# Performance work log

Hardware: AMD Instinct MI355X
Metric: run time of the kernel (lower is better)

## Reference

```python
import jax, jax.numpy as jnp
from jax import lax
import numpy as np

DIM = 256
QK = 256          # qk_dim defaults to dim
HEADS = 8
NWIN = 7
TOPK = 4
KS = 3            # side_dwconv


def setup_inputs() -> dict:
    key = jax.random.key(0)
    ks = jax.random.split(key, 8)
    B, H, W = 1, 112, 112
    s = lambda d: 1.0 / np.sqrt(d)
    return {
        "x": jax.random.normal(ks[0], (B, H, W, DIM), jnp.float32),
        # fused qkv linear: dim -> qk + qk + dim
        "w_qkv": jax.random.normal(ks[1], (DIM, 2 * QK + DIM), jnp.float32) * s(DIM),
        "b_qkv": jnp.zeros((2 * QK + DIM,), jnp.float32),
        # output projection
        "w_o": jax.random.normal(ks[2], (DIM, DIM), jnp.float32) * s(DIM),
        "b_o": jnp.zeros((DIM,), jnp.float32),
        # depthwise 3x3 lepe conv (HWIO with I=1, groups=dim)
        "lepe_w": jax.random.normal(ks[3], (KS, KS, 1, DIM), jnp.float32) * s(KS * KS),
        "lepe_b": jnp.zeros((DIM,), jnp.float32),
    }


def _win2img(t, B, H, W, c):
    # (B, p2, h, w, c) windows -> (B, H, W, c) image
    hw, ww = H // NWIN, W // NWIN
    t = t.reshape(B, NWIN, NWIN, hw, ww, c)
    return t.transpose(0, 1, 3, 2, 4, 5).reshape(B, H, W, c)


def reference(x, w_qkv, b_qkv, w_o, b_o, lepe_w, lepe_b):
    B, H, W, C = x.shape
    hw, ww = H // NWIN, W // NWIN
    p2, w2 = NWIN * NWIN, hw * ww
    hd_q, hd_v = QK // HEADS, DIM // HEADS
    scale = QK ** (-0.5)

    # partition into windows: (B, p2, hw, ww, C)
    xp = x.reshape(B, NWIN, hw, NWIN, ww, C).transpose(0, 1, 3, 2, 4, 5)
    xp = xp.reshape(B, p2, hw, ww, C)

    qkv = xp @ w_qkv + b_qkv
    q, kv = qkv[..., :QK], qkv[..., QK:]          # (B,p2,hw,ww,QK), (...,QK+DIM)

    q_pix = q.reshape(B, p2, w2, QK)
    kv_pix = kv.reshape(B, p2, w2, QK + DIM)      # identity kv_down

    # region-level routing (detached in original since diff_routing=False)
    q_win = lax.stop_gradient(q.mean((2, 3)))     # (B,p2,QK)
    k_win = lax.stop_gradient(kv[..., :QK].mean((2, 3)))
    logit = (q_win * scale) @ jnp.swapaxes(k_win, -1, -2)   # (B,p2,p2)
    top_logit, top_idx = lax.top_k(logit, TOPK)             # (B,p2,TOPK)
    r_weight = jax.nn.softmax(top_logit, axis=-1)           # unused: mul_weight='none'

    # gather top-k regions' KV: (B, p2, TOPK, w2, QK+DIM)
    kv_sel = jax.vmap(lambda kvb, idxb: kvb[idxb])(kv_pix, top_idx)

    k_sel = kv_sel[..., :QK].reshape(B, p2, TOPK * w2, HEADS, hd_q)
    v_sel = kv_sel[..., QK:].reshape(B, p2, TOPK * w2, HEADS, hd_v)
    qh = q_pix.reshape(B, p2, w2, HEADS, hd_q)

    attn = jnp.einsum('bpqhc,bpkhc->bphqk', qh * scale, k_sel)
    attn = jax.nn.softmax(attn, axis=-1)
    out = jnp.einsum('bphqk,bpkhc->bpqhc', attn, v_sel).reshape(B, p2, hw, ww, DIM)
    out = _win2img(out, B, H, W, DIM)

    # lepe: depthwise conv over v in image layout
    v_img = _win2img(kv[..., QK:], B, H, W, DIM)
    lepe = lax.conv_general_dilated(
        v_img, lepe_w, (1, 1), 'SAME',
        dimension_numbers=('NHWC', 'HWIO', 'NHWC'),
        feature_group_count=DIM) + lepe_b

    return (out + lepe) @ w_o + b_o
```

## Files before the change

kernel.cpp:

```cpp
#include <hip/hip_runtime.h>
#include <math.h>


typedef __bf16 bf16x8 __attribute__((ext_vector_type(8)));
typedef __bf16 bf16x4 __attribute__((ext_vector_type(4)));
typedef float f32x4 __attribute__((ext_vector_type(4)));

__global__ __launch_bounds__(64)
void pack1(const float* __restrict__ x, const float* __restrict__ w_qkv,
           const float* __restrict__ w_o, __bf16* __restrict__ xbf,
           __bf16* __restrict__ wtq, __bf16* __restrict__ wto) {
    const int b = blockIdx.x;
    const int t = threadIdx.x;
    if (b < 12544) {
        int p = b >> 8, pix = b & 255;
        int hh = (p / 7) * 16 + (pix >> 4);
        int ww = (p % 7) * 16 + (pix & 15);
        const float* src = x + ((size_t)(hh * 112 + ww)) * 256 + t * 4;
        float4 v = *(const float4*)src;
        bf16x4 o;
        o[0] = (__bf16)v.x; o[1] = (__bf16)v.y; o[2] = (__bf16)v.z; o[3] = (__bf16)v.w;
        *(bf16x4*)(xbf + (size_t)b * 256 + t * 4) = o;
    } else if (b < 12544 + 768) {
        int n = b - 12544;
        int k = t * 4;
        bf16x4 o;
        o[0] = (__bf16)w_qkv[(k + 0) * 768 + n];
        o[1] = (__bf16)w_qkv[(k + 1) * 768 + n];
        o[2] = (__bf16)w_qkv[(k + 2) * 768 + n];
        o[3] = (__bf16)w_qkv[(k + 3) * 768 + n];
        *(bf16x4*)(wtq + (size_t)n * 256 + k) = o;
    } else {
        int n = b - 12544 - 768;
        int k = t * 4;
        bf16x4 o;
        o[0] = (__bf16)w_o[(k + 0) * 256 + n];
        o[1] = (__bf16)w_o[(k + 1) * 256 + n];
        o[2] = (__bf16)w_o[(k + 2) * 256 + n];
        o[3] = (__bf16)w_o[(k + 3) * 256 + n];
        *(bf16x4*)(wto + (size_t)n * 256 + k) = o;
    }
}

template<int QKV>
__global__ __launch_bounds__(256)
void gemm_bf16(const __bf16* __restrict__ A,
               const __bf16* __restrict__ Wt,
               const float* __restrict__ bias,
               float* __restrict__ C, int N,
               __bf16* __restrict__ Qp,
               __bf16* __restrict__ Kp,
               __bf16* __restrict__ vbf,
               __bf16* __restrict__ Vt) {
    const int t = threadIdx.x & 63;
    const int wv = threadIdx.x >> 6;
    const int l16 = t & 15, quad = t >> 4;
    const int m0 = blockIdx.x * 64;
    const int n0 = blockIdx.y * 128 + wv * 32;

    __shared__ __bf16 Vs[128][72];

    f32x4 acc[2][4];
#pragma unroll
    for (int km = 0; km < 2; km++)
#pragma unroll
        for (int nt = 0; nt < 4; nt++) acc[km][nt] = (f32x4){0.f, 0.f, 0.f, 0.f};

#pragma unroll
    for (int ks = 0; ks < 8; ks++) {
        bf16x8 Af[2], Bf[4];
#pragma unroll
        for (int km = 0; km < 2; km++)
            Af[km] = *(const bf16x8*)(Wt + (size_t)(n0 + km * 16 + l16) * 256 + ks * 32 + quad * 8);
#pragma unroll
        for (int nt = 0; nt < 4; nt++)
            Bf[nt] = *(const bf16x8*)(A + (size_t)(m0 + nt * 16 + l16) * 256 + ks * 32 + quad * 8);
#pragma unroll
        for (int km = 0; km < 2; km++)
#pragma unroll
            for (int nt = 0; nt < 4; nt++)
                acc[km][nt] = __builtin_amdgcn_mfma_f32_16x16x32_bf16(
                    Af[km], Bf[nt], acc[km][nt], 0, 0, 0);
    }

#pragma unroll
    for (int km = 0; km < 2; km++) {
        const int n = n0 + km * 16 + quad * 4;
        float4 b4 = *(const float4*)(bias + n);
#pragma unroll
        for (int nt = 0; nt < 4; nt++) {
            const int m = m0 + nt * 16 + l16;
            float v0 = acc[km][nt][0] + b4.x;
            float v1 = acc[km][nt][1] + b4.y;
            float v2 = acc[km][nt][2] + b4.z;
            float v3 = acc[km][nt][3] + b4.w;
            if (QKV == 0) {
                float4 o = {v0, v1, v2, v3};
                *(float4*)(C + (size_t)m * N + n) = o;
            } else {
                const int p = m >> 8, pix = m & 255;
                if (n0 < 256) {
                    const float s = 1.4426950408889634f / 16.0f;
                    int h = n >> 5, cc = n & 31;
                    bf16x4 o;
                    o[0] = (__bf16)(v0 * s); o[1] = (__bf16)(v1 * s);
                    o[2] = (__bf16)(v2 * s); o[3] = (__bf16)(v3 * s);
                    *(bf16x4*)(Qp + ((size_t)((p * 8 + h) * 256 + pix)) * 32 + cc) = o;
                } else if (n0 < 512) {
                    int n2 = n - 256;
                    int h = n2 >> 5, cc = n2 & 31;
                    bf16x4 o;
                    o[0] = (__bf16)v0; o[1] = (__bf16)v1;
                    o[2] = (__bf16)v2; o[3] = (__bf16)v3;
                    *(bf16x4*)(Kp + ((size_t)((p * 8 + h) * 256 + pix)) * 32 + cc) = o;
                } else {
                    int n2 = n - 512;
                    int imgrow = ((p / 7) * 16 + (pix >> 4)) * 112 + (p % 7) * 16 + (pix & 15);
                    bf16x4 o;
                    o[0] = (__bf16)v0; o[1] = (__bf16)v1;
                    o[2] = (__bf16)v2; o[3] = (__bf16)v3;
                    *(bf16x4*)(vbf + (size_t)imgrow * 256 + n2) = o;
                    const int cbase = wv * 32 + km * 16 + quad * 4;
                    const int pb = nt * 16 + l16;
                    Vs[cbase + 0][pb] = o[0];
                    Vs[cbase + 1][pb] = o[1];
                    Vs[cbase + 2][pb] = o[2];
                    Vs[cbase + 3][pb] = o[3];
                }
            }
        }
    }

    if (QKV == 1 && blockIdx.y >= 4) {
        __syncthreads();
        const int p_ = m0 >> 8, qt_ = (m0 >> 6) & 3;
        const int vb = blockIdx.y * 128 - 512;
#pragma unroll
        for (int rep = 0; rep < 4; rep++) {
            int id = rep * 256 + threadIdx.x;
            int row = id >> 3, c8 = (id & 7) * 8;
            int hh = (vb + row) >> 5, c32 = (vb + row) & 31;
            bf16x8 val = *(const bf16x8*)&Vs[row][c8];
            *(bf16x8*)(Vt + ((size_t)((p_ * 8 + hh) * 32 + c32)) * 256 + qt_ * 64 + c8) = val;
        }
    }
}

__global__ __launch_bounds__(256)
void win_means(const __bf16* __restrict__ Qp,
               const __bf16* __restrict__ Kp,
               float* __restrict__ q_win, float* __restrict__ k_win) {
    const int b = blockIdx.x;
    const int p = b >> 3, h = b & 7;
    const int t = threadIdx.x;
    const int c8 = (t & 3) * 8;
    const int r0 = t >> 2;
    float aq[8], ak[8];
#pragma unroll
    for (int j = 0; j < 8; j++) { aq[j] = 0.f; ak[j] = 0.f; }
#pragma unroll
    for (int rg = 0; rg < 4; rg++) {
        const int r = rg * 64 + r0;
        bf16x8 q = *(const bf16x8*)(Qp + ((size_t)(b * 256 + r)) * 32 + c8);
        bf16x8 k = *(const bf16x8*)(Kp + ((size_t)(b * 256 + r)) * 32 + c8);
#pragma unroll
        for (int j = 0; j < 8; j++) { aq[j] += (float)q[j]; ak[j] += (float)k[j]; }
    }
    __shared__ float Sq[256][8], Sk[256][8];
#pragma unroll
    for (int j = 0; j < 8; j++) { Sq[t][j] = aq[j]; Sk[t][j] = ak[j]; }
    __syncthreads();
    if (t < 32) {
        const int grp = t >> 3, cj = t & 7;
        float sq = 0.f, sk = 0.f;
        for (int i = 0; i < 64; i++) {
            sq += Sq[i * 4 + grp][cj];
            sk += Sk[i * 4 + grp][cj];
        }
        q_win[p * 256 + h * 32 + t] = sq * (1.f / 256.f);
        k_win[p * 256 + h * 32 + t] = sk * (1.f / 256.f);
    }
}

__global__ __launch_bounds__(64)
void routing_topk(const float* __restrict__ q_win,
                  const float* __restrict__ k_win,
                  int* __restrict__ top_idx) {
    const int r = blockIdx.x;
    const int j = threadIdx.x;
    __shared__ float vals[64];

    float d = -1e30f;
    if (j < 49) {
        const float4* qp = (const float4*)(q_win + r * 256);
        const float4* kp = (const float4*)(k_win + j * 256);
        float s = 0.f;
#pragma unroll
        for (int c = 0; c < 64; c++) {
            float4 a = qp[c], b = kp[c];
            s += a.x * b.x + a.y * b.y + a.z * b.z + a.w * b.w;
        }
        d = s;
    }
    vals[j] = d;
    __syncthreads();
    if (j == 0) {
        float bv0 = -1e30f, bv1 = -1e30f, bv2 = -1e30f, bv3 = -1e30f;
        int bi0 = 0, bi1 = 0, bi2 = 0, bi3 = 0;
        for (int q = 0; q < 49; q++) {
            float v = vals[q];
            if (v > bv0) {
                bv3 = bv2; bi3 = bi2; bv2 = bv1; bi2 = bi1; bv1 = bv0; bi1 = bi0;
                bv0 = v; bi0 = q;
            } else if (v > bv1) {
                bv3 = bv2; bi3 = bi2; bv2 = bv1; bi2 = bi1; bv1 = v; bi1 = q;
            } else if (v > bv2) {
                bv3 = bv2; bi3 = bi2; bv2 = v; bi2 = q;
            } else if (v > bv3) {
                bv3 = v; bi3 = q;
            }
        }
        top_idx[r * 4 + 0] = bi0;
        top_idx[r * 4 + 1] = bi1;
        top_idx[r * 4 + 2] = bi2;
        top_idx[r * 4 + 3] = bi3;
    }
}

#define PLDS_PITCH 68
#define HALO_PITCH 36

__global__ __launch_bounds__(256)
void attn_mfma(const __bf16* __restrict__ Qp,
               const __bf16* __restrict__ Kp,
               const __bf16* __restrict__ Vt,
               const int* __restrict__ top_idx,
               const __bf16* __restrict__ vbf,
               const float* __restrict__ lw,
               const float* __restrict__ lb,
               __bf16* __restrict__ prebf) {
    const int bb = blockIdx.x;
    const int qt = bb / 392;
    const int ph = bb - qt * 392;
    const int p = ph >> 3;
    const int h = ph & 7;
    const int t = threadIdx.x & 63;
    const int wv = threadIdx.x >> 6;
    const int l16 = t & 15, quad = t >> 4;

    __shared__ union {
        unsigned short Plds[4][64 * PLDS_PITCH];
        struct {
            f32x4 O[4][2][4][64];
            float l[4][4][64];
        } red;
    } U;
    __shared__ __bf16 Hs[108 * HALO_PITCH];

    unsigned short* const Pw = U.Plds[wv];

    bf16x8 Qf[4];
#pragma unroll
    for (int nt = 0; nt < 4; nt++)
        Qf[nt] = *(const bf16x8*)(Qp + ((size_t)((p * 8 + h) * 256 + qt * 64 + nt * 16 + l16)) * 32 + quad * 8);

    const int sel = top_idx[p * 4 + wv];
    const __bf16* const Kb = Kp + ((size_t)(sel * 8 + h)) * 8192;
    const __bf16* const Vb = Vt + ((size_t)(sel * 8 + h)) * 8192;

    float lstate[4] = {0.f, 0.f, 0.f, 0.f};
    f32x4 O[2][4];
#pragma unroll
    for (int mt = 0; mt < 2; mt++)
#pragma unroll
        for (int nt = 0; nt < 4; nt++) O[mt][nt] = (f32x4){0.f, 0.f, 0.f, 0.f};

    bf16x8 Kf[4];
#pragma unroll
    for (int km = 0; km < 4; km++)
        Kf[km] = *(const bf16x8*)(Kb + (size_t)(km * 16 + l16) * 32 + quad * 8);

    for (int kc = 0; kc < 4; kc++) {
        const int kbase = kc * 64;

        bf16x8 Vf[2][2];
#pragma unroll
        for (int ks = 0; ks < 2; ks++)
#pragma unroll
            for (int mt = 0; mt < 2; mt++)
                Vf[ks][mt] = *(const bf16x8*)(Vb + (size_t)(mt * 16 + l16) * 256 + kbase + ks * 32 + quad * 8);

        const int kbn = (kc < 3 ? kc + 1 : 3) * 64;
        bf16x8 Kn[4];
#pragma unroll
        for (int km = 0; km < 4; km++)
            Kn[km] = *(const bf16x8*)(Kb + (size_t)(kbn + km * 16 + l16) * 32 + quad * 8);

#pragma unroll
        for (int nt = 0; nt < 4; nt++) {
            f32x4 S[4];
#pragma unroll
            for (int km = 0; km < 4; km++)
                S[km] = __builtin_amdgcn_mfma_f32_16x16x32_bf16(
                    Kf[km], Qf[nt], (f32x4){0.f, 0.f, 0.f, 0.f}, 0, 0, 0);

            float rs = 0.f;
#pragma unroll
            for (int km = 0; km < 4; km++) {
                union { unsigned short u[4]; ushort4 v; } pk;
#pragma unroll
                for (int r = 0; r < 4; r++) {
                    float pv = __builtin_amdgcn_exp2f(S[km][r]);
                    rs += pv;
                    pk.u[r] = __builtin_bit_cast(unsigned short, (__bf16)pv);
                }
                *(ushort4*)&Pw[(nt * 16 + l16) * PLDS_PITCH + km * 16 + quad * 4] = pk.v;
            }
            rs += __shfl_xor(rs, 16);
            rs += __shfl_xor(rs, 32);
            lstate[nt] += rs;
        }

#pragma unroll
        for (int ks = 0; ks < 2; ks++) {
#pragma unroll
            for (int nt = 0; nt < 4; nt++) {
                int idx = (nt * 16 + l16) * PLDS_PITCH + ks * 32 + quad * 8;
                union { ushort4 u4[2]; bf16x8 v; } pu;
                pu.u4[0] = *(const ushort4*)&Pw[idx];
                pu.u4[1] = *(const ushort4*)&Pw[idx + 4];
#pragma unroll
                for (int mt = 0; mt < 2; mt++)
                    O[mt][nt] = __builtin_amdgcn_mfma_f32_16x16x32_bf16(
                        Vf[ks][mt], pu.v, O[mt][nt], 0, 0, 0);
            }
        }

#pragma unroll
        for (int km = 0; km < 4; km++) Kf[km] = Kn[km];
    }

    __syncthreads();
#pragma unroll
    for (int mt = 0; mt < 2; mt++)
#pragma unroll
        for (int nt = 0; nt < 4; nt++)
            U.red.O[wv][mt][nt][t] = O[mt][nt];
#pragma unroll
    for (int nt = 0; nt < 4; nt++)
        U.red.l[wv][nt][t] = lstate[nt];

    const int pr = p / 7, pc = p % 7;
    if (threadIdx.x < 108) {
        const int i = threadIdx.x;
        int hy = i / 18, hx = i - hy * 18;
        int gy = pr * 16 + qt * 4 - 1 + hy;
        int gx = pc * 16 - 1 + hx;
        union { bf16x4 v4[8]; bf16x8 v8[4]; uint4 q[4]; } u;
        u.q[0] = (uint4){0u, 0u, 0u, 0u};
        u.q[1] = (uint4){0u, 0u, 0u, 0u};
        u.q[2] = (uint4){0u, 0u, 0u, 0u};
        u.q[3] = (uint4){0u, 0u, 0u, 0u};
        if (gy >= 0 && gy < 112 && gx >= 0 && gx < 112) {
            const __bf16* src = vbf + ((size_t)(gy * 112 + gx)) * 256 + h * 32;
            u.v8[0] = *(const bf16x8*)src;
            u.v8[1] = *(const bf16x8*)(src + 8);
            u.v8[2] = *(const bf16x8*)(src + 16);
            u.v8[3] = *(const bf16x8*)(src + 24);
        }
#pragma unroll
        for (int j = 0; j < 8; j++)
            *(bf16x4*)&Hs[i * HALO_PITCH + j * 4] = u.v4[j];
    }
    __syncthreads();

    const int nt = wv;
    const float ltot = U.red.l[0][nt][t] + U.red.l[1][nt][t]
                     + U.red.l[2][nt][t] + U.red.l[3][nt][t];
    const float inv = 1.f / ltot;
    const int himg = pr * 16 + qt * 4 + nt, wimg = pc * 16 + l16;
#pragma unroll
    for (int mt = 0; mt < 2; mt++) {
        f32x4 o = U.red.O[0][mt][nt][t];
#pragma unroll
        for (int v = 1; v < 4; v++) {
            f32x4 ov = U.red.O[v][mt][nt][t];
            o[0] += ov[0]; o[1] += ov[1]; o[2] += ov[2]; o[3] += ov[3];
        }
        const int c = h * 32 + mt * 16 + quad * 4;
        const float4 lbv = *(const float4*)(lb + c);
        float a0 = lbv.x, a1 = lbv.y, a2 = lbv.z, a3 = lbv.w;
#pragma unroll
        for (int dh = 0; dh < 3; dh++)
#pragma unroll
            for (int dw = 0; dw < 3; dw++) {
                const float4 w4 = *(const float4*)(lw + (dh * 3 + dw) * 256 + c);
                const bf16x4 v4 = *(const bf16x4*)&Hs[((nt + dh) * 18 + l16 + dw) * HALO_PITCH + mt * 16 + quad * 4];
                a0 += (float)v4[0] * w4.x;
                a1 += (float)v4[1] * w4.y;
                a2 += (float)v4[2] * w4.z;
                a3 += (float)v4[3] * w4.w;
            }
        bf16x4 ob;
        ob[0] = (__bf16)(o[0] * inv + a0);
        ob[1] = (__bf16)(o[1] * inv + a1);
        ob[2] = (__bf16)(o[2] * inv + a2);
        ob[3] = (__bf16)(o[3] * inv + a3);
        *(bf16x4*)(prebf + ((size_t)(himg * 112 + wimg)) * 256 + c) = ob;
    }
}

extern "C" void kernel_launch(void* const* d_in, const int* in_sizes, int n_in,
                              void* d_out, int out_size, void* d_ws, size_t ws_size,
                              hipStream_t stream) {
    const float* x      = (const float*)d_in[0];
    const float* w_qkv  = (const float*)d_in[1];
    const float* b_qkv  = (const float*)d_in[2];
    const float* w_o    = (const float*)d_in[3];
    const float* b_o    = (const float*)d_in[4];
    const float* lepe_w = (const float*)d_in[5];
    const float* lepe_b = (const float*)d_in[6];
    float* out = (float*)d_out;

    char* w = (char*)d_ws;
    __bf16* Qp    = (__bf16*)w; w += 6422528;
    __bf16* Kp    = (__bf16*)w; w += 6422528;
    __bf16* vbf   = (__bf16*)w; w += 6422528;
    __bf16* Vt    = (__bf16*)w; w += 6422528;
    __bf16* xbf   = (__bf16*)w;
    __bf16* prebf = (__bf16*)w; w += 6422528;
    __bf16* wtq   = (__bf16*)w; w += 393216;
    __bf16* wto   = (__bf16*)w; w += 131072;
    float* q_win   = (float*)w; w += 12544 * 4;
    float* k_win   = (float*)w; w += 12544 * 4;
    int*   top_idx = (int*)w;

    pack1<<<12544 + 768 + 256, 64, 0, stream>>>(x, w_qkv, w_o, xbf, wtq, wto);
    gemm_bf16<1><<<dim3(196, 6), 256, 0, stream>>>(xbf, wtq, b_qkv,
                                                   nullptr, 0, Qp, Kp, vbf, Vt);
    win_means<<<392, 256, 0, stream>>>(Qp, Kp, q_win, k_win);
    routing_topk<<<49, 64, 0, stream>>>(q_win, k_win, top_idx);
    attn_mfma<<<392 * 4, 256, 0, stream>>>(Qp, Kp, Vt, top_idx,
                                           vbf, lepe_w, lepe_b, prebf);
    gemm_bf16<0><<<dim3(196, 2), 256, 0, stream>>>(prebf, wto, b_o,
                                                   out, 256, nullptr, nullptr, nullptr, nullptr);
}
```

Baseline: 183.0 us.

## Drop LDS halo staging for lepe conv and add MFMA priority hints

```diff
diff --git a/kernel.cpp b/kernel.cpp
--- a/kernel.cpp
+++ b/kernel.cpp
@@ -228,7 +228,6 @@
 }
 
 #define PLDS_PITCH 68
-#define HALO_PITCH 36
 
 __global__ __launch_bounds__(256)
 void attn_mfma(const __bf16* __restrict__ Qp,
@@ -255,7 +254,6 @@
             float l[4][4][64];
         } red;
     } U;
-    __shared__ __bf16 Hs[108 * HALO_PITCH];
 
     unsigned short* const Pw = U.Plds[wv];
 
@@ -299,10 +297,12 @@
 #pragma unroll
         for (int nt = 0; nt < 4; nt++) {
             f32x4 S[4];
+            __builtin_amdgcn_s_setprio(1);
 #pragma unroll
             for (int km = 0; km < 4; km++)
                 S[km] = __builtin_amdgcn_mfma_f32_16x16x32_bf16(
                     Kf[km], Qf[nt], (f32x4){0.f, 0.f, 0.f, 0.f}, 0, 0, 0);
+            __builtin_amdgcn_s_setprio(0);
 
             float rs = 0.f;
 #pragma unroll
@@ -329,10 +329,12 @@
                 union { ushort4 u4[2]; bf16x8 v; } pu;
                 pu.u4[0] = *(const ushort4*)&Pw[idx];
                 pu.u4[1] = *(const ushort4*)&Pw[idx + 4];
+                __builtin_amdgcn_s_setprio(1);
 #pragma unroll
                 for (int mt = 0; mt < 2; mt++)
                     O[mt][nt] = __builtin_amdgcn_mfma_f32_16x16x32_bf16(
                         Vf[ks][mt], pu.v, O[mt][nt], 0, 0, 0);
+                __builtin_amdgcn_s_setprio(0);
             }
         }
 
@@ -349,31 +351,9 @@
 #pragma unroll
     for (int nt = 0; nt < 4; nt++)
         U.red.l[wv][nt][t] = lstate[nt];
+    __syncthreads();
 
     const int pr = p / 7, pc = p % 7;
-    if (threadIdx.x < 108) {
-        const int i = threadIdx.x;
-        int hy = i / 18, hx = i - hy * 18;
-        int gy = pr * 16 + qt * 4 - 1 + hy;
-        int gx = pc * 16 - 1 + hx;
-        union { bf16x4 v4[8]; bf16x8 v8[4]; uint4 q[4]; } u;
-        u.q[0] = (uint4){0u, 0u, 0u, 0u};
-        u.q[1] = (uint4){0u, 0u, 0u, 0u};
-        u.q[2] = (uint4){0u, 0u, 0u, 0u};
-        u.q[3] = (uint4){0u, 0u, 0u, 0u};
-        if (gy >= 0 && gy < 112 && gx >= 0 && gx < 112) {
-            const __bf16* src = vbf + ((size_t)(gy * 112 + gx)) * 256 + h * 32;
-            u.v8[0] = *(const bf16x8*)src;
-            u.v8[1] = *(const bf16x8*)(src + 8);
-            u.v8[2] = *(const bf16x8*)(src + 16);
-            u.v8[3] = *(const bf16x8*)(src + 24);
-        }
-#pragma unroll
-        for (int j = 0; j < 8; j++)
-            *(bf16x4*)&Hs[i * HALO_PITCH + j * 4] = u.v4[j];
-    }
-    __syncthreads();
-
     const int nt = wv;
     const float ltot = U.red.l[0][nt][t] + U.red.l[1][nt][t]
                      + U.red.l[2][nt][t] + U.red.l[3][nt][t];
@@ -388,19 +368,33 @@
             o[0] += ov[0]; o[1] += ov[1]; o[2] += ov[2]; o[3] += ov[3];
         }
         const int c = h * 32 + mt * 16 + quad * 4;
+
+        bf16x4 tap[9];
+#pragma unroll
+        for (int dh = 0; dh < 3; dh++) {
+            const int gy = himg - 1 + dh;
+#pragma unroll
+            for (int dw = 0; dw < 3; dw++) {
+                const int gx = wimg - 1 + dw;
+                bf16x4 v4;
+                v4[0] = (__bf16)0.f; v4[1] = (__bf16)0.f;
+                v4[2] = (__bf16)0.f; v4[3] = (__bf16)0.f;
+                if (gy >= 0 && gy < 112 && gx >= 0 && gx < 112)
+                    v4 = *(const bf16x4*)(vbf + ((size_t)(gy * 112 + gx)) * 256 + c);
+                tap[dh * 3 + dw] = v4;
+            }
+        }
+
         const float4 lbv = *(const float4*)(lb + c);
         float a0 = lbv.x, a1 = lbv.y, a2 = lbv.z, a3 = lbv.w;
 #pragma unroll
-        for (int dh = 0; dh < 3; dh++)
-#pragma unroll
-            for (int dw = 0; dw < 3; dw++) {
-                const float4 w4 = *(const float4*)(lw + (dh * 3 + dw) * 256 + c);
-                const bf16x4 v4 = *(const bf16x4*)&Hs[((nt + dh) * 18 + l16 + dw) * HALO_PITCH + mt * 16 + quad * 4];
-                a0 += (float)v4[0] * w4.x;
-                a1 += (float)v4[1] * w4.y;
-                a2 += (float)v4[2] * w4.z;
-                a3 += (float)v4[3] * w4.w;
-            }
+        for (int k = 0; k < 9; k++) {
+            const float4 w4 = *(const float4*)(lw + k * 256 + c);
+            a0 += (float)tap[k][0] * w4.x;
+            a1 += (float)tap[k][1] * w4.y;
+            a2 += (float)tap[k][2] * w4.z;
+            a3 += (float)tap[k][3] * w4.w;
+        }
         bf16x4 ob;
         ob[0] = (__bf16)(o[0] * inv + a0);
         ob[1] = (__bf16)(o[1] * inv + a1);
```

Measured after the change: 194.1 us. 1.06x slower.

## Fuse input conversion and window means into QKV GEMM, add MFMA priority hints

Applied to the files above, without the earlier changes.

```diff
diff --git a/kernel.cpp b/kernel.cpp
--- a/kernel.cpp
+++ b/kernel.cpp
@@ -7,22 +7,13 @@
 typedef float f32x4 __attribute__((ext_vector_type(4)));
 
 __global__ __launch_bounds__(64)
-void pack1(const float* __restrict__ x, const float* __restrict__ w_qkv,
-           const float* __restrict__ w_o, __bf16* __restrict__ xbf,
-           __bf16* __restrict__ wtq, __bf16* __restrict__ wto) {
+void pack1(const float* __restrict__ w_qkv, const float* __restrict__ w_o,
+           __bf16* __restrict__ wtq, __bf16* __restrict__ wto,
+           float* __restrict__ qkwin) {
     const int b = blockIdx.x;
     const int t = threadIdx.x;
-    if (b < 12544) {
-        int p = b >> 8, pix = b & 255;
-        int hh = (p / 7) * 16 + (pix >> 4);
-        int ww = (p % 7) * 16 + (pix & 15);
-        const float* src = x + ((size_t)(hh * 112 + ww)) * 256 + t * 4;
-        float4 v = *(const float4*)src;
-        bf16x4 o;
-        o[0] = (__bf16)v.x; o[1] = (__bf16)v.y; o[2] = (__bf16)v.z; o[3] = (__bf16)v.w;
-        *(bf16x4*)(xbf + (size_t)b * 256 + t * 4) = o;
-    } else if (b < 12544 + 768) {
-        int n = b - 12544;
+    if (b < 768) {
+        int n = b;
         int k = t * 4;
         bf16x4 o;
         o[0] = (__bf16)w_qkv[(k + 0) * 768 + n];
@@ -30,8 +21,8 @@
         o[2] = (__bf16)w_qkv[(k + 2) * 768 + n];
         o[3] = (__bf16)w_qkv[(k + 3) * 768 + n];
         *(bf16x4*)(wtq + (size_t)n * 256 + k) = o;
-    } else {
-        int n = b - 12544 - 768;
+    } else if (b < 1024) {
+        int n = b - 768;
         int k = t * 4;
         bf16x4 o;
         o[0] = (__bf16)w_o[(k + 0) * 256 + n];
@@ -39,19 +30,25 @@
         o[2] = (__bf16)w_o[(k + 2) * 256 + n];
         o[3] = (__bf16)w_o[(k + 3) * 256 + n];
         *(bf16x4*)(wto + (size_t)n * 256 + k) = o;
+    } else {
+        int idx = (b - 1024) * 64 + t;
+        *(float4*)(qkwin + (size_t)idx * 4) = (float4){0.f, 0.f, 0.f, 0.f};
     }
 }
 
 template<int QKV>
 __global__ __launch_bounds__(256)
 void gemm_bf16(const __bf16* __restrict__ A,
+               const float* __restrict__ Ax,
                const __bf16* __restrict__ Wt,
                const float* __restrict__ bias,
                float* __restrict__ C, int N,
                __bf16* __restrict__ Qp,
                __bf16* __restrict__ Kp,
                __bf16* __restrict__ vbf,
-               __bf16* __restrict__ Vt) {
+               __bf16* __restrict__ Vt,
+               float* __restrict__ q_win,
+               float* __restrict__ k_win) {
     const int t = threadIdx.x & 63;
     const int wv = threadIdx.x >> 6;
     const int l16 = t & 15, quad = t >> 4;
@@ -60,6 +57,18 @@
 
     __shared__ __bf16 Vs[128][72];
 
+    int mrow[4];
+#pragma unroll
+    for (int nt = 0; nt < 4; nt++) {
+        const int m = m0 + nt * 16 + l16;
+        if (QKV == 1) {
+            const int p = m >> 8, pix = m & 255;
+            mrow[nt] = ((p / 7) * 16 + (pix >> 4)) * 112 + (p % 7) * 16 + (pix & 15);
+        } else {
+            mrow[nt] = m;
+        }
+    }
+
     f32x4 acc[2][4];
 #pragma unroll
     for (int km = 0; km < 2; km++)
@@ -73,8 +82,21 @@
         for (int km = 0; km < 2; km++)
             Af[km] = *(const bf16x8*)(Wt + (size_t)(n0 + km * 16 + l16) * 256 + ks * 32 + quad * 8);
 #pragma unroll
-        for (int nt = 0; nt < 4; nt++)
-            Bf[nt] = *(const bf16x8*)(A + (size_t)(m0 + nt * 16 + l16) * 256 + ks * 32 + quad * 8);
+        for (int nt = 0; nt < 4; nt++) {
+            if (QKV == 1) {
+                const float* s = Ax + (size_t)mrow[nt] * 256 + ks * 32 + quad * 8;
+                const float4 f0 = *(const float4*)s;
+                const float4 f1 = *(const float4*)(s + 4);
+                bf16x8 bv;
+                bv[0] = (__bf16)f0.x; bv[1] = (__bf16)f0.y;
+                bv[2] = (__bf16)f0.z; bv[3] = (__bf16)f0.w;
+                bv[4] = (__bf16)f1.x; bv[5] = (__bf16)f1.y;
+                bv[6] = (__bf16)f1.z; bv[7] = (__bf16)f1.w;
+                Bf[nt] = bv;
+            } else {
+                Bf[nt] = *(const bf16x8*)(A + (size_t)mrow[nt] * 256 + ks * 32 + quad * 8);
+            }
+        }
 #pragma unroll
         for (int km = 0; km < 2; km++)
 #pragma unroll
@@ -82,6 +104,12 @@
                 acc[km][nt] = __builtin_amdgcn_mfma_f32_16x16x32_bf16(
                     Af[km], Bf[nt], acc[km][nt], 0, 0, 0);
     }
+
+    float ws[2][4];
+#pragma unroll
+    for (int km = 0; km < 2; km++)
+#pragma unroll
+        for (int j = 0; j < 4; j++) ws[km][j] = 0.f;
 
 #pragma unroll
     for (int km = 0; km < 2; km++) {
@@ -99,6 +127,10 @@
                 *(float4*)(C + (size_t)m * N + n) = o;
             } else {
                 const int p = m >> 8, pix = m & 255;
+                if (n0 < 512) {
+                    ws[km][0] += v0; ws[km][1] += v1;
+                    ws[km][2] += v2; ws[km][3] += v3;
+                }
                 if (n0 < 256) {
                     const float s = 1.4426950408889634f / 16.0f;
                     int h = n >> 5, cc = n & 31;
@@ -131,6 +163,31 @@
         }
     }
 
+    if (QKV == 1 && n0 < 512) {
+        const int pblk = m0 >> 8;
+#pragma unroll
+        for (int km = 0; km < 2; km++) {
+#pragma unroll
+            for (int j = 0; j < 4; j++) {
+                float s = ws[km][j];
+                s += __shfl_xor(s, 1);
+                s += __shfl_xor(s, 2);
+                s += __shfl_xor(s, 4);
+                s += __shfl_xor(s, 8);
+                ws[km][j] = s;
+            }
+            if (l16 == 0) {
+                const int n = n0 + km * 16 + quad * 4;
+                float* dst = (n < 256) ? (q_win + pblk * 256 + n)
+                                       : (k_win + pblk * 256 + (n - 256));
+                atomicAdd(dst + 0, ws[km][0]);
+                atomicAdd(dst + 1, ws[km][1]);
+                atomicAdd(dst + 2, ws[km][2]);
+                atomicAdd(dst + 3, ws[km][3]);
+            }
+        }
+    }
+
     if (QKV == 1 && blockIdx.y >= 4) {
         __syncthreads();
         const int p_ = m0 >> 8, qt_ = (m0 >> 6) & 3;
@@ -143,42 +200,6 @@
             bf16x8 val = *(const bf16x8*)&Vs[row][c8];
             *(bf16x8*)(Vt + ((size_t)((p_ * 8 + hh) * 32 + c32)) * 256 + qt_ * 64 + c8) = val;
         }
-    }
-}
-
-__global__ __launch_bounds__(256)
-void win_means(const __bf16* __restrict__ Qp,
-               const __bf16* __restrict__ Kp,
-               float* __restrict__ q_win, float* __restrict__ k_win) {
-    const int b = blockIdx.x;
-    const int p = b >> 3, h = b & 7;
-    const int t = threadIdx.x;
-    const int c8 = (t & 3) * 8;
-    const int r0 = t >> 2;
-    float aq[8], ak[8];
-#pragma unroll
-    for (int j = 0; j < 8; j++) { aq[j] = 0.f; ak[j] = 0.f; }
-#pragma unroll
-    for (int rg = 0; rg < 4; rg++) {
-        const int r = rg * 64 + r0;
-        bf16x8 q = *(const bf16x8*)(Qp + ((size_t)(b * 256 + r)) * 32 + c8);
-        bf16x8 k = *(const bf16x8*)(Kp + ((size_t)(b * 256 + r)) * 32 + c8);
-#pragma unroll
-        for (int j = 0; j < 8; j++) { aq[j] += (float)q[j]; ak[j] += (float)k[j]; }
-    }
-    __shared__ float Sq[256][8], Sk[256][8];
-#pragma unroll
-    for (int j = 0; j < 8; j++) { Sq[t][j] = aq[j]; Sk[t][j] = ak[j]; }
-    __syncthreads();
-    if (t < 32) {
-        const int grp = t >> 3, cj = t & 7;
-        float sq = 0.f, sk = 0.f;
-        for (int i = 0; i < 64; i++) {
-            sq += Sq[i * 4 + grp][cj];
-            sk += Sk[i * 4 + grp][cj];
-        }
-        q_win[p * 256 + h * 32 + t] = sq * (1.f / 256.f);
-        k_win[p * 256 + h * 32 + t] = sk * (1.f / 256.f);
     }
 }
 
@@ -299,10 +320,12 @@
 #pragma unroll
         for (int nt = 0; nt < 4; nt++) {
             f32x4 S[4];
+            __builtin_amdgcn_s_setprio(1);
 #pragma unroll
             for (int km = 0; km < 4; km++)
                 S[km] = __builtin_amdgcn_mfma_f32_16x16x32_bf16(
                     Kf[km], Qf[nt], (f32x4){0.f, 0.f, 0.f, 0.f}, 0, 0, 0);
+            __builtin_amdgcn_s_setprio(0);
 
             float rs = 0.f;
 #pragma unroll
@@ -329,10 +352,12 @@
                 union { ushort4 u4[2]; bf16x8 v; } pu;
                 pu.u4[0] = *(const ushort4*)&Pw[idx];
                 pu.u4[1] = *(const ushort4*)&Pw[idx + 4];
+                __builtin_amdgcn_s_setprio(1);
 #pragma unroll
                 for (int mt = 0; mt < 2; mt++)
                     O[mt][nt] = __builtin_amdgcn_mfma_f32_16x16x32_bf16(
                         Vf[ks][mt], pu.v, O[mt][nt], 0, 0, 0);
+                __builtin_amdgcn_s_setprio(0);
             }
         }
 
@@ -427,7 +452,6 @@
     __bf16* Kp    = (__bf16*)w; w += 6422528;
     __bf16* vbf   = (__bf16*)w; w += 6422528;
     __bf16* Vt    = (__bf16*)w; w += 6422528;
-    __bf16* xbf   = (__bf16*)w;
     __bf16* prebf = (__bf16*)w; w += 6422528;
     __bf16* wtq   = (__bf16*)w; w += 393216;
     __bf16* wto   = (__bf16*)w; w += 131072;
@@ -435,13 +459,14 @@
     float* k_win   = (float*)w; w += 12544 * 4;
     int*   top_idx = (int*)w;
 
-    pack1<<<12544 + 768 + 256, 64, 0, stream>>>(x, w_qkv, w_o, xbf, wtq, wto);
-    gemm_bf16<1><<<dim3(196, 6), 256, 0, stream>>>(xbf, wtq, b_qkv,
-                                                   nullptr, 0, Qp, Kp, vbf, Vt);
-    win_means<<<392, 256, 0, stream>>>(Qp, Kp, q_win, k_win);
+    pack1<<<768 + 256 + 98, 64, 0, stream>>>(w_qkv, w_o, wtq, wto, q_win);
+    gemm_bf16<1><<<dim3(196, 6), 256, 0, stream>>>(nullptr, x, wtq, b_qkv,
+                                                   nullptr, 0, Qp, Kp, vbf, Vt,
+                                                   q_win, k_win);
     routing_topk<<<49, 64, 0, stream>>>(q_win, k_win, top_idx);
     attn_mfma<<<392 * 4, 256, 0, stream>>>(Qp, Kp, Vt, top_idx,
                                            vbf, lepe_w, lepe_b, prebf);
-    gemm_bf16<0><<<dim3(196, 2), 256, 0, stream>>>(prebf, wto, b_o,
-                                                   out, 256, nullptr, nullptr, nullptr, nullptr);
+    gemm_bf16<0><<<dim3(196, 2), 256, 0, stream>>>(prebf, nullptr, wto, b_o,
+                                                   out, 256, nullptr, nullptr, nullptr, nullptr,
+                                                   nullptr, nullptr);
 }
```

Result: slower. 192.7 us (+5.3%).
